# Kernel tuning notes

Hardware: AMD Instinct MI355X
Metric: run time of the kernel (lower is better)

The kernel has to match this reference:

```python
import jax, jax.numpy as jnp
import numpy as np

B, S, H = 64, 2048, 1024
INPUT_SCALE = 100.0
DT = 0.01


def setup_inputs() -> dict:
    key = jax.random.key(0)
    ks = jax.random.split(key, 16)
    def vec(k, scale=0.5):
        return jax.random.normal(k, (H,), jnp.float32) * scale
    x_codes = 65.0 + 10.0 * jax.random.normal(ks[0], (B, S), jnp.float32)
    return {
        "x_codes": x_codes,
        "Wi_w": vec(ks[1]), "Wi_b": vec(ks[2], 0.1),
        "Wf_w": vec(ks[3]), "Wf_b": vec(ks[4], 0.1),
        "Wo_w": vec(ks[5]), "Wo_b": vec(ks[6], 0.1),
        "Wg_w": vec(ks[7]), "Wg_b": vec(ks[8], 0.1),
        "Wl_w": vec(ks[9]), "Wl_b": vec(ks[10], 0.1),
        "proj_w": jax.random.normal(ks[11], (2, H), jnp.float32) * 0.03,
        "proj_b": jnp.zeros((2,), jnp.float32),
        "n_init": jnp.zeros((H,), jnp.float32),
    }


def reference(x_codes, Wi_w, Wi_b, Wf_w, Wf_b, Wo_w, Wo_b, Wg_w, Wg_b,
              Wl_w, Wl_b, proj_w, proj_b, n_init):
    b, s = x_codes.shape
    h0 = jnp.zeros((b, H), x_codes.dtype)
    c0 = jnp.zeros_like(h0)
    n0 = jnp.broadcast_to(n_init, (b, H))
    x = (x_codes - 65.0) / INPUT_SCALE          # [B,S]
    xs = x.T[:, :, None]                         # [S,B,1] scan over time

    def step(carry, xt):
        h, c, n = carry
        pre_i = xt * Wi_w + Wi_b                 # [B,H] (Linear(1,H))
        pre_f = xt * Wf_w + Wf_b
        pre_o = xt * Wo_w + Wo_b
        pre_g = xt * Wg_w + Wg_b
        lam = jax.nn.sigmoid(xt * Wl_w + Wl_b)
        i_t = jnp.exp(pre_i - n)
        f_t = jnp.exp(pre_f - n)
        o_t = jnp.exp(pre_o - n)
        g_t = jax.nn.sigmoid(pre_g)              # act_g == 'sigmoid'
        c_new = f_t * c + i_t * g_t
        ff = o_t * jax.nn.sigmoid(c_new)         # act_c == 'sigmoid'
        h_new = (h + DT * ff) / (1.0 + DT * lam)
        n_new = n + 0.01 * (i_t + f_t + o_t - 3.0)
        y = h_new @ proj_w.T + proj_b            # [B,2]
        return (h_new, c_new, n_new), y

    _, ys = jax.lax.scan(step, (h0, c0, n0), xs)  # ys: [S,B,2]
    return ys.transpose(1, 0, 2)                  # [B,S,2]
```

## Files before the change

kernel.cpp:

```cpp
#include <hip/hip_runtime.h>


#define Bv   64
#define Sv   2048
#define Hv   1024
#define TPB  256
#define NT   512
#define CH   16
#define HSTR 17
#define HBUF (TPB * HSTR)

#define L2E   1.44269504088896340736f
#define NL2E (-1.44269504088896340736f)
#define LN2   0.69314718055994530942f
#define KNU   0.014426950408889634f
#define CREB  0.692493619626702435f
#define LOG2_001 (-6.6438561897747247f)

__device__ __forceinline__ float fexp2(float x) { return __builtin_amdgcn_exp2f(x); }
__device__ __forceinline__ float frcp(float x)  { return __builtin_amdgcn_rcpf(x); }

__global__ __launch_bounds__(256) void init_out(const float* __restrict__ proj_b,
                                                float* __restrict__ out) {
    int i = blockIdx.x * 256 + threadIdx.x;
    out[i] = proj_b[i & 1];
}

__global__ __launch_bounds__(NT, 1) void cfc_scan(
    const float* __restrict__ x_codes,
    const float* __restrict__ Wi_w, const float* __restrict__ Wi_b,
    const float* __restrict__ Wf_w, const float* __restrict__ Wf_b,
    const float* __restrict__ Wo_w, const float* __restrict__ Wo_b,
    const float* __restrict__ Wg_w, const float* __restrict__ Wg_b,
    const float* __restrict__ Wl_w, const float* __restrict__ Wl_b,
    const float* __restrict__ proj_w,
    const float* __restrict__ n_init,
    float* __restrict__ out)
{
    __shared__ float hlds[2 * HBUF];
    __shared__ float pwlds[2 * TPB];

    const int b   = blockIdx.x >> 2;
    const int q   = blockIdx.x & 3;
    const int tid = threadIdx.x;

    const float* __restrict__ xrow = x_codes + b * Sv;
    float* __restrict__ orow = out + b * (Sv * 2);

    const int ct   = tid - TPB;
    const int rk   = (ct >> 7) & 1;
    const int rt   = (ct >> 3) & 15;
    const int rseg = ct & 7;
    if (tid >= TPB) {
        pwlds[ct]       = proj_w[q * TPB + ct];
        pwlds[TPB + ct] = proj_w[Hv + q * TPB + ct];
    }

    float wi2 = 0, bi2 = 0, wf2 = 0, bf2 = 0, wo2 = 0, bo2 = 0;
    float wg2 = 0, bg2 = 0, wl2 = 0, bl2 = 0;
    float m = 0, En = 0, C = 0, h = 0;
    if (tid < TPB) {
        const int j = q * TPB + tid;
        const float wi = Wi_w[j], bi = Wi_b[j];
        const float wf = Wf_w[j], bf = Wf_b[j];
        const float wo = Wo_w[j], bo = Wo_b[j];
        const float wg = Wg_w[j], bg = Wg_b[j];
        const float wl = Wl_w[j], bl = Wl_b[j];
        wi2 = wi * KNU;  bi2 = fmaf(-0.65f, wi, bi) * L2E;
        wf2 = wf * KNU;  bf2 = fmaf(-0.65f, wf, bf) * L2E;
        wo2 = wo * KNU;  bo2 = fmaf(-0.65f, wo, bo) * L2E + LOG2_001;
        wg2 = -wg * KNU; bg2 = fmaf(-0.65f, wg, bg) * NL2E;
        wl2 = -wl * KNU; bl2 = fmaf(-0.65f, wl, bl) * NL2E;
        m  = n_init[j] * NL2E;
        En = fexp2(m);
    }

    float Gf[CH], GiGg[CH], Goa[CH], Gs[CH], Il[CH];

    static const float CUP[CH] = {
        1.0f,        1.03045453f, 1.06183655f, 1.09417428f,
        1.12749685f, 1.16183424f, 1.19721736f, 1.23367806f,
        1.27124915f, 1.30996445f, 1.34985881f, 1.39096813f,
        1.43332941f, 1.47698079f, 1.52196156f, 1.56831219f };

    int par = 0;
    for (int t0 = 0; t0 < Sv; t0 += CH, par ^= 1) {
        if (tid < TPB) {
            #pragma unroll
            for (int u = 0; u < CH; ++u) {
                const float xc = xrow[t0 + u];
                const float Gi = fexp2(fmaf(xc, wi2, bi2));
                Gf[u]  = fexp2(fmaf(xc, wf2, bf2));
                Goa[u] = fexp2(fmaf(xc, wo2, bo2));
                const float eg = fexp2(fmaf(xc, wg2, bg2));
                const float Gg = frcp(fmaf(eg, -LN2, -LN2));
                GiGg[u] = Gi * Gg;
                const float el = fexp2(fmaf(xc, wl2, bl2));
                Il[u]   = fmaf(frcp(el + 1.01f), -0.01f, 1.0f);
                Gs[u]   = fmaf(Goa[u], 100.0f, Gi + Gf[u]);
            }
            float* __restrict__ hrow = &hlds[par * HBUF + tid * HSTR];
            #pragma unroll
            for (int u = 0; u < CH; ++u) {
                const float Enu = (u == 0) ? En : En * CUP[u];
                const float ef  = Gf[u] * Enu;
                C = fmaf(ef, C, GiGg[u] * Enu);
                const float sc = frcp(1.0f + fexp2(C));
                h = fmaf(Goa[u] * Enu, sc, h) * Il[u];
                hrow[u] = h;
                m = fmaf(Gs[u] * Enu, -KNU, m);
                if (u == CH - 1) m += CREB;
                En = fexp2(m);
            }
        }
        __syncthreads();
        if (tid >= TPB) {
            const float* __restrict__ hb  = &hlds[par * HBUF];
            const float* __restrict__ pwk = &pwlds[rk * TPB];
            float sum = 0.0f;
            #pragma unroll
            for (int i2 = 0; i2 < 32; ++i2) {
                const int v  = (i2 + 4 * rseg) & 31;
                const int jj = rseg * 32 + v;
                sum = fmaf(hb[jj * HSTR + rt], pwk[jj], sum);
            }
            sum += __shfl_xor(sum, 1, 64);
            sum += __shfl_xor(sum, 2, 64);
            sum += __shfl_xor(sum, 4, 64);
            if (rseg == 0) atomicAdd(&orow[(t0 + rt) * 2 + rk], sum);
        }
    }
}

extern "C" void kernel_launch(void* const* d_in, const int* in_sizes, int n_in,
                              void* d_out, int out_size, void* d_ws, size_t ws_size,
                              hipStream_t stream) {
    const float* x_codes = (const float*)d_in[0];
    const float* Wi_w = (const float*)d_in[1];
    const float* Wi_b = (const float*)d_in[2];
    const float* Wf_w = (const float*)d_in[3];
    const float* Wf_b = (const float*)d_in[4];
    const float* Wo_w = (const float*)d_in[5];
    const float* Wo_b = (const float*)d_in[6];
    const float* Wg_w = (const float*)d_in[7];
    const float* Wg_b = (const float*)d_in[8];
    const float* Wl_w = (const float*)d_in[9];
    const float* Wl_b = (const float*)d_in[10];
    const float* proj_w = (const float*)d_in[11];
    const float* proj_b = (const float*)d_in[12];
    const float* n_init = (const float*)d_in[13];
    float* out = (float*)d_out;

    init_out<<<out_size / 256, 256, 0, stream>>>(proj_b, out);
    cfc_scan<<<Bv * (Hv / TPB), NT, 0, stream>>>(
        x_codes, Wi_w, Wi_b, Wf_w, Wf_b, Wo_w, Wo_b, Wg_w, Wg_b, Wl_w, Wl_b,
        proj_w, n_init, out);
}
```

Before: 275.7 us.

## Software-pipeline gate computation and split recurrence into C/m pass and h pass

Computes the input-dependent gate values for the next chunk while the current chunk's recurrence finishes, so transcendental work overlaps with the serial dependency chain. The loop is split: one pass advances only C and the normaliser m (the critical chain), and a second pass computes the sigmoid of C and the h update. Paired reciprocals (one rcp of a product shared across two values) cut the number of rcp instructions for the gate sigmoid, lambda and the C sigmoid. The ln2 factor is folded into the input-gate bias. This raises register pressure with more per-chunk arrays, and the extra gate pass on the final chunk reads a wrapped-around index that is discarded.

```diff
diff --git a/kernel.cpp b/kernel.cpp
--- a/kernel.cpp
+++ b/kernel.cpp
@@ -16,6 +16,7 @@
 #define KNU   0.014426950408889634f
 #define CREB  0.692493619626702435f
 #define LOG2_001 (-6.6438561897747247f)
+#define LOG2_L2E 0.52876637294489777f
 
 __device__ __forceinline__ float fexp2(float x) { return __builtin_amdgcn_exp2f(x); }
 __device__ __forceinline__ float frcp(float x)  { return __builtin_amdgcn_rcpf(x); }
@@ -25,6 +26,30 @@
     int i = blockIdx.x * 256 + threadIdx.x;
     out[i] = proj_b[i & 1];
 }
+
+#define GATES_MAIN(tb)                                                \
+    _Pragma("unroll")                                                 \
+    for (int u = 0; u < CH; ++u) {                                    \
+        const float xc = xrow[(tb) + u];                              \
+        const float gi = fexp2(fmaf(xc, wi2, bi2));  \
+        const float gf = fexp2(fmaf(xc, wf2, bf2));  \
+        const float go = fexp2(fmaf(xc, wo2, bo2));  \
+        const float eg = fexp2(fmaf(xc, wg2, bg2));  \
+        const float el = fexp2(fmaf(xc, wl2, bl2));  \
+        const float Aq = 1.0f + eg;                                   \
+        const float Bq = 1.01f + el;                                  \
+        const float rq = frcp(Aq * Bq);      \
+        gF[u]  = gf;                                                  \
+        gOa[u] = go;                                                  \
+        gIG[u] = gi * (rq * Bq);      \
+        rA[u]  = rq * Aq;             \
+        gS[u]  = fmaf(go, 100.0f, fmaf(gi, LN2, gf)); \
+    }
+
+#define GATES_IL()                                                    \
+    _Pragma("unroll")                                                 \
+    for (int u = 0; u < CH; ++u)                                      \
+        gIl[u] = fmaf(rA[u], -0.01f, 1.0f);
 
 __global__ __launch_bounds__(NT, 1) void cfc_scan(
     const float* __restrict__ x_codes,
@@ -66,7 +91,7 @@
         const float wo = Wo_w[j], bo = Wo_b[j];
         const float wg = Wg_w[j], bg = Wg_b[j];
         const float wl = Wl_w[j], bl = Wl_b[j];
-        wi2 = wi * KNU;  bi2 = fmaf(-0.65f, wi, bi) * L2E;
+        wi2 = wi * KNU;  bi2 = fmaf(-0.65f, wi, bi) * L2E + LOG2_L2E;
         wf2 = wf * KNU;  bf2 = fmaf(-0.65f, wf, bf) * L2E;
         wo2 = wo * KNU;  bo2 = fmaf(-0.65f, wo, bo) * L2E + LOG2_001;
         wg2 = -wg * KNU; bg2 = fmaf(-0.65f, wg, bg) * NL2E;
@@ -75,7 +100,8 @@
         En = fexp2(m);
     }
 
-    float Gf[CH], GiGg[CH], Goa[CH], Gs[CH], Il[CH];
+    float gF[CH], gIG[CH], gOa[CH], gS[CH], gIl[CH], rA[CH];
+    float Carr[CH], Pa[CH];
 
     static const float CUP[CH] = {
         1.0f,        1.03045453f, 1.06183655f, 1.09417428f,
@@ -83,35 +109,39 @@
         1.27124915f, 1.30996445f, 1.34985881f, 1.39096813f,
         1.43332941f, 1.47698079f, 1.52196156f, 1.56831219f };
 
+    if (tid < TPB) {
+        GATES_MAIN(0)
+        GATES_IL()
+    }
+
     int par = 0;
     for (int t0 = 0; t0 < Sv; t0 += CH, par ^= 1) {
         if (tid < TPB) {
             #pragma unroll
             for (int u = 0; u < CH; ++u) {
-                const float xc = xrow[t0 + u];
-                const float Gi = fexp2(fmaf(xc, wi2, bi2));
-                Gf[u]  = fexp2(fmaf(xc, wf2, bf2));
-                Goa[u] = fexp2(fmaf(xc, wo2, bo2));
-                const float eg = fexp2(fmaf(xc, wg2, bg2));
-                const float Gg = frcp(fmaf(eg, -LN2, -LN2));
-                GiGg[u] = Gi * Gg;
-                const float el = fexp2(fmaf(xc, wl2, bl2));
-                Il[u]   = fmaf(frcp(el + 1.01f), -0.01f, 1.0f);
-                Gs[u]   = fmaf(Goa[u], 100.0f, Gi + Gf[u]);
-            }
-            float* __restrict__ hrow = &hlds[par * HBUF + tid * HSTR];
-            #pragma unroll
-            for (int u = 0; u < CH; ++u) {
                 const float Enu = (u == 0) ? En : En * CUP[u];
-                const float ef  = Gf[u] * Enu;
-                C = fmaf(ef, C, GiGg[u] * Enu);
-                const float sc = frcp(1.0f + fexp2(C));
-                h = fmaf(Goa[u] * Enu, sc, h) * Il[u];
-                hrow[u] = h;
-                m = fmaf(Gs[u] * Enu, -KNU, m);
+                const float ef  = gF[u] * Enu;
+                C = fmaf(ef, C, -(gIG[u] * Enu));
+                Carr[u] = C;
+                Pa[u]   = gOa[u] * Enu;
+                m = fmaf(gS[u] * Enu, -KNU, m);
                 if (u == CH - 1) m += CREB;
                 En = fexp2(m);
             }
+            const int tnext = (t0 + CH) & (Sv - 1);
+            GATES_MAIN(tnext)
+            float* __restrict__ hrow = &hlds[par * HBUF + tid * HSTR];
+            #pragma unroll
+            for (int u = 0; u < CH; u += 2) {
+                const float A0 = 1.0f + fexp2(Carr[u]);
+                const float A1 = 1.0f + fexp2(Carr[u + 1]);
+                const float rr = frcp(A0 * A1);
+                h = fmaf(Pa[u],     rr * A1, h) * gIl[u];
+                hrow[u] = h;
+                h = fmaf(Pa[u + 1], rr * A0, h) * gIl[u + 1];
+                hrow[u + 1] = h;
+            }
+            GATES_IL()
         }
         __syncthreads();
         if (tid >= TPB) {
```

New measurement: 276.2 us. Within noise of the previous version (+0.2%).

## Offload gate precompute to helper waves and pipeline with the recurrence

Applied to the files above, without the earlier changes.

The second half of the block (helper threads) now computes the i/f/o/g gate exponentials for the next chunk into double-buffered LDS as packed float4s, while the recurrence threads consume the current chunk. The projection reduction is deferred by one chunk, and proj_w is held in registers. The recurrence is split into a serial C/m pass followed by a paired sigmoid pass that shares one reciprocal across two steps. The chunk size is halved to 8 and the h layout is transposed. The aim is to take transcendental work off the serial critical path, at the cost of more LDS traffic and more barriers per timestep.

```diff
diff --git a/kernel.cpp b/kernel.cpp
--- a/kernel.cpp
+++ b/kernel.cpp
@@ -6,16 +6,21 @@
 #define Hv   1024
 #define TPB  256
 #define NT   512
-#define CH   16
-#define HSTR 17
-#define HBUF (TPB * HSTR)
+#define CH   8
+#define NCHUNK (Sv / CH)
+#define GSTR 36
+#define GBUF (TPB * GSTR)
+#define HROW 293
+#define HBUF2 (CH * HROW)
 
 #define L2E   1.44269504088896340736f
 #define NL2E (-1.44269504088896340736f)
 #define LN2   0.69314718055994530942f
 #define KNU   0.014426950408889634f
-#define CREB  0.692493619626702435f
+#define NKNU (-0.014426950408889634f)
+#define CREB8 0.34624680981335122f
 #define LOG2_001 (-6.6438561897747247f)
+#define LOG2_L2E 0.52876637294489777f
 
 __device__ __forceinline__ float fexp2(float x) { return __builtin_amdgcn_exp2f(x); }
 __device__ __forceinline__ float frcp(float x)  { return __builtin_amdgcn_rcpf(x); }
@@ -25,6 +30,40 @@
     int i = blockIdx.x * 256 + threadIdx.x;
     out[i] = proj_b[i & 1];
 }
+
+#define GATE_TILE(dstbase, tb)                                          \
+    {                                                                   \
+        float* __restrict__ gw = (dstbase);                             \
+        _Pragma("unroll")                                               \
+        for (int u = 0; u < CH; ++u) {                                  \
+            const float xc = xrow[(tb) + u];                            \
+            const float gi = fexp2(fmaf(xc, wi2, bi2));   \
+            const float gf = fexp2(fmaf(xc, wf2, bf2));   \
+            const float go = fexp2(fmaf(xc, wo2, bo2));   \
+            const float eg = fexp2(fmaf(xc, wg2, bg2));   \
+            const float rg = frcp(1.0f + eg);             \
+            float4 v;                                                   \
+            v.x = gf;                                                   \
+            v.y = gi * rg;                                              \
+            v.z = go;                                                   \
+            v.w = fmaf(go, NL2E, fmaf(gi, -0.01f, gf * NKNU));          \
+            *reinterpret_cast<float4*>(gw + 4 * u) = v;                 \
+        }                                                               \
+    }
+
+#define PROJ_REDUCE(hbase, tglob)                                       \
+    {                                                                   \
+        const float* __restrict__ hb = (hbase);                         \
+        float sum = 0.0f;                                               \
+        _Pragma("unroll")                                               \
+        for (int i2 = 0; i2 < 16; ++i2)                                 \
+            sum = fmaf(hb[i2], pwr[i2], sum);                           \
+        sum += __shfl_xor(sum, 1, 64);                                  \
+        sum += __shfl_xor(sum, 2, 64);                                  \
+        sum += __shfl_xor(sum, 4, 64);                                  \
+        sum += __shfl_xor(sum, 8, 64);                                  \
+        if (rseg == 0) atomicAdd(&orow[(tglob) * 2 + rk], sum);         \
+    }
 
 __global__ __launch_bounds__(NT, 1) void cfc_scan(
     const float* __restrict__ x_codes,
@@ -37,8 +76,8 @@
     const float* __restrict__ n_init,
     float* __restrict__ out)
 {
-    __shared__ float hlds[2 * HBUF];
-    __shared__ float pwlds[2 * TPB];
+    __shared__ __align__(16) float glds[2 * GBUF];
+    __shared__ float hlds[2 * HBUF2];
 
     const int b   = blockIdx.x >> 2;
     const int q   = blockIdx.x & 3;
@@ -47,88 +86,93 @@
     const float* __restrict__ xrow = x_codes + b * Sv;
     float* __restrict__ orow = out + b * (Sv * 2);
 
-    const int ct   = tid - TPB;
-    const int rk   = (ct >> 7) & 1;
-    const int rt   = (ct >> 3) & 15;
-    const int rseg = ct & 7;
-    if (tid >= TPB) {
-        pwlds[ct]       = proj_w[q * TPB + ct];
-        pwlds[TPB + ct] = proj_w[Hv + q * TPB + ct];
-    }
-
     float wi2 = 0, bi2 = 0, wf2 = 0, bf2 = 0, wo2 = 0, bo2 = 0;
     float wg2 = 0, bg2 = 0, wl2 = 0, bl2 = 0;
     float m = 0, En = 0, C = 0, h = 0;
-    if (tid < TPB) {
-        const int j = q * TPB + tid;
+    float pwr[16];
+    int   rk = 0, rt = 0, rseg = 0, wtid = 0;
+
+    static const float CUP[CH] = {
+        1.0f,        1.03045453f, 1.06183655f, 1.09417428f,
+        1.12749685f, 1.16183424f, 1.19721736f, 1.23367806f };
+
+    if (tid >= TPB) {
+        const int ct = tid - TPB;
+        const int j  = q * TPB + ct;
         const float wi = Wi_w[j], bi = Wi_b[j];
         const float wf = Wf_w[j], bf = Wf_b[j];
         const float wo = Wo_w[j], bo = Wo_b[j];
         const float wg = Wg_w[j], bg = Wg_b[j];
-        const float wl = Wl_w[j], bl = Wl_b[j];
-        wi2 = wi * KNU;  bi2 = fmaf(-0.65f, wi, bi) * L2E;
+        wi2 = wi * KNU;  bi2 = fmaf(-0.65f, wi, bi) * L2E + LOG2_L2E;
         wf2 = wf * KNU;  bf2 = fmaf(-0.65f, wf, bf) * L2E;
         wo2 = wo * KNU;  bo2 = fmaf(-0.65f, wo, bo) * L2E + LOG2_001;
         wg2 = -wg * KNU; bg2 = fmaf(-0.65f, wg, bg) * NL2E;
+        rk   = ct >> 7;
+        rt   = (ct >> 4) & 7;
+        rseg = ct & 15;
+        #pragma unroll
+        for (int i2 = 0; i2 < 16; ++i2)
+            pwr[i2] = proj_w[rk * Hv + q * TPB + rseg * 16 + i2];
+        GATE_TILE(&glds[ct * GSTR], 0)
+    } else {
+        const int j = q * TPB + tid;
+        const float wl = Wl_w[j], bl = Wl_b[j];
         wl2 = -wl * KNU; bl2 = fmaf(-0.65f, wl, bl) * NL2E;
         m  = n_init[j] * NL2E;
         En = fexp2(m);
-    }
-
-    float Gf[CH], GiGg[CH], Goa[CH], Gs[CH], Il[CH];
-
-    static const float CUP[CH] = {
-        1.0f,        1.03045453f, 1.06183655f, 1.09417428f,
-        1.12749685f, 1.16183424f, 1.19721736f, 1.23367806f,
-        1.27124915f, 1.30996445f, 1.34985881f, 1.39096813f,
-        1.43332941f, 1.47698079f, 1.52196156f, 1.56831219f };
+        wtid = tid + 2 * (tid >> 4);
+    }
+
+    __syncthreads();
 
     int par = 0;
-    for (int t0 = 0; t0 < Sv; t0 += CH, par ^= 1) {
+    for (int k = 0; k < NCHUNK; ++k, par ^= 1) {
         if (tid < TPB) {
+            const int t0 = k * CH;
+            const float* __restrict__ gp = &glds[par * GBUF + tid * GSTR];
+            float elv[CH], Carr[CH], Pa[CH];
+            #pragma unroll
+            for (int u = 0; u < CH; ++u)
+                elv[u] = fexp2(fmaf(xrow[t0 + u], wl2, bl2));
             #pragma unroll
             for (int u = 0; u < CH; ++u) {
-                const float xc = xrow[t0 + u];
-                const float Gi = fexp2(fmaf(xc, wi2, bi2));
-                Gf[u]  = fexp2(fmaf(xc, wf2, bf2));
-                Goa[u] = fexp2(fmaf(xc, wo2, bo2));
-                const float eg = fexp2(fmaf(xc, wg2, bg2));
-                const float Gg = frcp(fmaf(eg, -LN2, -LN2));
-                GiGg[u] = Gi * Gg;
-                const float el = fexp2(fmaf(xc, wl2, bl2));
-                Il[u]   = fmaf(frcp(el + 1.01f), -0.01f, 1.0f);
-                Gs[u]   = fmaf(Goa[u], 100.0f, Gi + Gf[u]);
+                const float4 g = *reinterpret_cast<const float4*>(gp + 4 * u);
+                const float Enu = En * CUP[u];
+                C = fmaf(g.x * Enu, C, -(g.y * Enu));
+                Carr[u] = C;
+                Pa[u]   = g.z * Enu;
+                m = fmaf(g.w, Enu, m);
+                if (u == CH - 1) m += CREB8;
+                En = fexp2(m);
             }
-            float* __restrict__ hrow = &hlds[par * HBUF + tid * HSTR];
+            float* __restrict__ hw = &hlds[par * HBUF2 + wtid];
             #pragma unroll
-            for (int u = 0; u < CH; ++u) {
-                const float Enu = (u == 0) ? En : En * CUP[u];
-                const float ef  = Gf[u] * Enu;
-                C = fmaf(ef, C, GiGg[u] * Enu);
-                const float sc = frcp(1.0f + fexp2(C));
-                h = fmaf(Goa[u] * Enu, sc, h) * Il[u];
-                hrow[u] = h;
-                m = fmaf(Gs[u] * Enu, -KNU, m);
-                if (u == CH - 1) m += CREB;
-                En = fexp2(m);
+            for (int p = 0; p < CH / 2; ++p) {
+                const float B0 = 1.01f + elv[2 * p];
+                const float B1 = 1.01f + elv[2 * p + 1];
+                const float rB = frcp(B0 * B1);
+                const float A0 = 1.0f + fexp2(Carr[2 * p]);
+                const float A1 = 1.0f + fexp2(Carr[2 * p + 1]);
+                const float rA = frcp(A0 * A1);
+                h = fmaf(Pa[2 * p], rA * A1, h) * fmaf(rB * B1, -0.01f, 1.0f);
+                hw[(2 * p) * HROW] = h;
+                h = fmaf(Pa[2 * p + 1], rA * A0, h) * fmaf(rB * B0, -0.01f, 1.0f);
+                hw[(2 * p + 1) * HROW] = h;
+            }
+        } else {
+            const int ct = tid - TPB;
+            const int tn = ((k + 1) & (NCHUNK - 1)) * CH;
+            GATE_TILE(&glds[(par ^ 1) * GBUF + ct * GSTR], tn)
+            if (k) {
+                PROJ_REDUCE(&hlds[(par ^ 1) * HBUF2 + rt * HROW + rseg * 18],
+                            (k - 1) * CH + rt)
             }
         }
         __syncthreads();
-        if (tid >= TPB) {
-            const float* __restrict__ hb  = &hlds[par * HBUF];
-            const float* __restrict__ pwk = &pwlds[rk * TPB];
-            float sum = 0.0f;
-            #pragma unroll
-            for (int i2 = 0; i2 < 32; ++i2) {
-                const int v  = (i2 + 4 * rseg) & 31;
-                const int jj = rseg * 32 + v;
-                sum = fmaf(hb[jj * HSTR + rt], pwk[jj], sum);
-            }
-            sum += __shfl_xor(sum, 1, 64);
-            sum += __shfl_xor(sum, 2, 64);
-            sum += __shfl_xor(sum, 4, 64);
-            if (rseg == 0) atomicAdd(&orow[(t0 + rt) * 2 + rk], sum);
-        }
+    }
+    if (tid >= TPB) {
+        PROJ_REDUCE(&hlds[HBUF2 + rt * HROW + rseg * 18],
+                    (NCHUNK - 1) * CH + rt)
     }
 }
 
```

After: 327.2 us. 1.19x slower.

## Software-pipeline gate precompute for the next chunk into the current chunk's recurrence

Applied to the files above, without the earlier changes.

Restructures the scan so the input-dependent gate exponentials for chunk k+1 are computed interleaved with the serial C/m recurrence of chunk k, using double-buffered register arrays and a manually unrolled two-chunk loop. The h update is split off, with the sigmoid(C) reciprocals paired into one rcp per two steps, and x values are prefetched two chunks ahead as float4 loads. Launch bounds change to allow two blocks per CU. The aim is to hide the latency of the transcendental-heavy precompute behind the dependent chain, at the cost of higher register pressure and more complex code.

```diff
diff --git a/kernel.cpp b/kernel.cpp
--- a/kernel.cpp
+++ b/kernel.cpp
@@ -16,6 +16,7 @@
 #define KNU   0.014426950408889634f
 #define CREB  0.692493619626702435f
 #define LOG2_001 (-6.6438561897747247f)
+#define LOG2_L2E 0.52876637294489777f
 
 __device__ __forceinline__ float fexp2(float x) { return __builtin_amdgcn_exp2f(x); }
 __device__ __forceinline__ float frcp(float x)  { return __builtin_amdgcn_rcpf(x); }
@@ -26,7 +27,85 @@
     out[i] = proj_b[i & 1];
 }
 
-__global__ __launch_bounds__(NT, 1) void cfc_scan(
+#define XCOMP(qv, v) ((v)==0?(qv).x:(v)==1?(qv).y:(v)==2?(qv).z:(qv).w)
+#define XGET(X, u)   XCOMP(X[(u) >> 2], (u) & 3)
+
+#define NG_FIN(w, NGF, NGIG, NGOA, NGS, NGIL)                                   \
+    NGF[w]  = sgf[w];                                                           \
+    NGOA[w] = sgo[w];                                                           \
+    NGIG[w] = sgi[w] * srg[w];                              \
+    NGIL[w] = fmaf(srl[w], -0.01f, 1.0f);                  \
+    NGS[w]  = fmaf(sgo[w], 100.0f, fmaf(sgi[w], LN2, sgf[w]));
+
+#define CONSUME_PROJ(T0, PAR)                                                   \
+    if (tid >= TPB) {                                                           \
+        const float* __restrict__ hb  = &hlds[(PAR) * HBUF];                    \
+        const float* __restrict__ pwk = &pwlds[rk * TPB];                       \
+        float sum = 0.0f;                                                       \
+        _Pragma("unroll")                                                       \
+        for (int i2 = 0; i2 < 32; ++i2) {                                       \
+            const int v  = (i2 + 4 * rseg) & 31;                                \
+            const int jj = rseg * 32 + v;                                       \
+            sum = fmaf(hb[jj * HSTR + rt], pwk[jj], sum);                       \
+        }                                                                       \
+        sum += __shfl_xor(sum, 1, 64);                                          \
+        sum += __shfl_xor(sum, 2, 64);                                          \
+        sum += __shfl_xor(sum, 4, 64);                                          \
+        if (rseg == 0) atomicAdd(&orow[((T0) + rt) * 2 + rk], sum);             \
+    }
+
+#define CHUNK_BODY(T0, PAR, CGF, CGIG, CGOA, CGS, CGIL,                         \
+                   NGF, NGIG, NGOA, NGS, NGIL, XU, XL)                          \
+    if (tid < TPB) {                                                            \
+        { const int tx = ((T0) + 2 * CH) & (Sv - 1);                            \
+          XL[0] = *reinterpret_cast<const float4*>(xrow + tx);                  \
+          XL[1] = *reinterpret_cast<const float4*>(xrow + tx + 4);              \
+          XL[2] = *reinterpret_cast<const float4*>(xrow + tx + 8);              \
+          XL[3] = *reinterpret_cast<const float4*>(xrow + tx + 12); }           \
+        float Carr[CH], Pa[CH], eA[CH];                                         \
+        float sgi[CH], sgf[CH], sgo[CH], seg[CH], sel[CH], srg[CH], srl[CH];    \
+        _Pragma("unroll")                                                       \
+        for (int u = 0; u < CH; ++u) {                                          \
+            const float EnN = fexp2(m);                        \
+            { const float xc = XGET(XU, u);       \
+              sgi[u] = fexp2(fmaf(xc, wi2, bi2));                               \
+              sgf[u] = fexp2(fmaf(xc, wf2, bf2));                               \
+              sgo[u] = fexp2(fmaf(xc, wo2, bo2));                               \
+              seg[u] = fexp2(fmaf(xc, wg2, bg2));                               \
+              sel[u] = fexp2(fmaf(xc, wl2, bl2)); }                             \
+            if (u >= 1) {                            \
+                srg[u-1] = frcp(1.0f  + seg[u-1]);                              \
+                srl[u-1] = frcp(1.01f + sel[u-1]);                              \
+                eA[u-1]  = fexp2(Carr[u-1]);                                    \
+            }                                                                   \
+            if (u >= 2) { NG_FIN(u-2, NGF, NGIG, NGOA, NGS, NGIL) }             \
+            { const float Enu = EnN * CUP[u];            \
+              const float ef  = CGF[u] * Enu;                                   \
+              C = fmaf(ef, C, -(CGIG[u] * Enu));                                \
+              Carr[u] = C;                                                      \
+              Pa[u]   = CGOA[u] * Enu;                                          \
+              m = fmaf(CGS[u] * Enu, -KNU, m); }                                \
+        }                                                                       \
+        m += CREB;                                            \
+        srg[CH-1] = frcp(1.0f  + seg[CH-1]);                  \
+        srl[CH-1] = frcp(1.01f + sel[CH-1]);                                    \
+        eA[CH-1]  = fexp2(Carr[CH-1]);                                          \
+        NG_FIN(CH-2, NGF, NGIG, NGOA, NGS, NGIL)                                \
+        float* __restrict__ hrow = &hlds[(PAR) * HBUF + tid * HSTR];            \
+        _Pragma("unroll")                                                       \
+        for (int p = 0; p < CH / 2; ++p) {                                      \
+            const float A0 = 1.0f + eA[2*p];            \
+            const float A1 = 1.0f + eA[2*p+1];                                  \
+            const float rr = frcp(A0 * A1);             \
+            h = fmaf(Pa[2*p],   rr * A1, h) * CGIL[2*p];   hrow[2*p]   = h;     \
+            h = fmaf(Pa[2*p+1], rr * A0, h) * CGIL[2*p+1]; hrow[2*p+1] = h;     \
+            if (p == 5) { NG_FIN(CH-1, NGF, NGIG, NGOA, NGS, NGIL) }            \
+        }                                                                       \
+    }                                                                           \
+    __syncthreads();                                                            \
+    CONSUME_PROJ(T0, PAR)
+
+__global__ __launch_bounds__(NT, 2) void cfc_scan(
     const float* __restrict__ x_codes,
     const float* __restrict__ Wi_w, const float* __restrict__ Wi_b,
     const float* __restrict__ Wf_w, const float* __restrict__ Wf_b,
@@ -58,7 +137,7 @@
 
     float wi2 = 0, bi2 = 0, wf2 = 0, bf2 = 0, wo2 = 0, bo2 = 0;
     float wg2 = 0, bg2 = 0, wl2 = 0, bl2 = 0;
-    float m = 0, En = 0, C = 0, h = 0;
+    float m = 0, C = 0, h = 0;
     if (tid < TPB) {
         const int j = q * TPB + tid;
         const float wi = Wi_w[j], bi = Wi_b[j];
@@ -66,16 +145,13 @@
         const float wo = Wo_w[j], bo = Wo_b[j];
         const float wg = Wg_w[j], bg = Wg_b[j];
         const float wl = Wl_w[j], bl = Wl_b[j];
-        wi2 = wi * KNU;  bi2 = fmaf(-0.65f, wi, bi) * L2E;
+        wi2 = wi * KNU;  bi2 = fmaf(-0.65f, wi, bi) * L2E + LOG2_L2E;
         wf2 = wf * KNU;  bf2 = fmaf(-0.65f, wf, bf) * L2E;
         wo2 = wo * KNU;  bo2 = fmaf(-0.65f, wo, bo) * L2E + LOG2_001;
         wg2 = -wg * KNU; bg2 = fmaf(-0.65f, wg, bg) * NL2E;
         wl2 = -wl * KNU; bl2 = fmaf(-0.65f, wl, bl) * NL2E;
         m  = n_init[j] * NL2E;
-        En = fexp2(m);
-    }
-
-    float Gf[CH], GiGg[CH], Goa[CH], Gs[CH], Il[CH];
+    }
 
     static const float CUP[CH] = {
         1.0f,        1.03045453f, 1.06183655f, 1.09417428f,
@@ -83,52 +159,41 @@
         1.27124915f, 1.30996445f, 1.34985881f, 1.39096813f,
         1.43332941f, 1.47698079f, 1.52196156f, 1.56831219f };
 
-    int par = 0;
-    for (int t0 = 0; t0 < Sv; t0 += CH, par ^= 1) {
-        if (tid < TPB) {
+    float GAf[CH], GAig[CH], GAoa[CH], GAs[CH], GAil[CH];
+    float GBf[CH], GBig[CH], GBoa[CH], GBs[CH], GBil[CH];
+    float4 xA[4], xB[4];
+
+    if (tid < TPB) {
+        #pragma unroll
+        for (int u4 = 0; u4 < 4; ++u4) {
+            const float4 xq = *reinterpret_cast<const float4*>(xrow + 4 * u4);
             #pragma unroll
-            for (int u = 0; u < CH; ++u) {
-                const float xc = xrow[t0 + u];
-                const float Gi = fexp2(fmaf(xc, wi2, bi2));
-                Gf[u]  = fexp2(fmaf(xc, wf2, bf2));
-                Goa[u] = fexp2(fmaf(xc, wo2, bo2));
+            for (int v = 0; v < 4; ++v) {
+                const int u = 4 * u4 + v;
+                const float xc = XCOMP(xq, v);
+                const float gi = fexp2(fmaf(xc, wi2, bi2));
+                const float gf = fexp2(fmaf(xc, wf2, bf2));
+                const float go = fexp2(fmaf(xc, wo2, bo2));
                 const float eg = fexp2(fmaf(xc, wg2, bg2));
-                const float Gg = frcp(fmaf(eg, -LN2, -LN2));
-                GiGg[u] = Gi * Gg;
                 const float el = fexp2(fmaf(xc, wl2, bl2));
-                Il[u]   = fmaf(frcp(el + 1.01f), -0.01f, 1.0f);
-                Gs[u]   = fmaf(Goa[u], 100.0f, Gi + Gf[u]);
-            }
-            float* __restrict__ hrow = &hlds[par * HBUF + tid * HSTR];
-            #pragma unroll
-            for (int u = 0; u < CH; ++u) {
-                const float Enu = (u == 0) ? En : En * CUP[u];
-                const float ef  = Gf[u] * Enu;
-                C = fmaf(ef, C, GiGg[u] * Enu);
-                const float sc = frcp(1.0f + fexp2(C));
-                h = fmaf(Goa[u] * Enu, sc, h) * Il[u];
-                hrow[u] = h;
-                m = fmaf(Gs[u] * Enu, -KNU, m);
-                if (u == CH - 1) m += CREB;
-                En = fexp2(m);
+                GAf[u]  = gf;
+                GAoa[u] = go;
+                GAig[u] = gi * frcp(1.0f + eg);
+                GAil[u] = fmaf(frcp(1.01f + el), -0.01f, 1.0f);
+                GAs[u]  = fmaf(go, 100.0f, fmaf(gi, LN2, gf));
             }
         }
-        __syncthreads();
-        if (tid >= TPB) {
-            const float* __restrict__ hb  = &hlds[par * HBUF];
-            const float* __restrict__ pwk = &pwlds[rk * TPB];
-            float sum = 0.0f;
-            #pragma unroll
-            for (int i2 = 0; i2 < 32; ++i2) {
-                const int v  = (i2 + 4 * rseg) & 31;
-                const int jj = rseg * 32 + v;
-                sum = fmaf(hb[jj * HSTR + rt], pwk[jj], sum);
-            }
-            sum += __shfl_xor(sum, 1, 64);
-            sum += __shfl_xor(sum, 2, 64);
-            sum += __shfl_xor(sum, 4, 64);
-            if (rseg == 0) atomicAdd(&orow[(t0 + rt) * 2 + rk], sum);
-        }
+        xA[0] = *reinterpret_cast<const float4*>(xrow + CH);
+        xA[1] = *reinterpret_cast<const float4*>(xrow + CH + 4);
+        xA[2] = *reinterpret_cast<const float4*>(xrow + CH + 8);
+        xA[3] = *reinterpret_cast<const float4*>(xrow + CH + 12);
+    }
+
+    for (int t0 = 0; t0 < Sv; t0 += 2 * CH) {
+        CHUNK_BODY(t0,      0, GAf, GAig, GAoa, GAs, GAil,
+                               GBf, GBig, GBoa, GBs, GBil, xA, xB)
+        CHUNK_BODY(t0 + CH, 1, GBf, GBig, GBoa, GBs, GBil,
+                               GAf, GAig, GAoa, GAs, GAil, xB, xA)
     }
 }
 
```

Result: slower. 445.6 us (+61.6%).
